# Optimization experiments

Measured on AMD Instinct MI355X. Metric: run time of the kernel, lower is better.

Reference implementation:

```python
import jax, jax.numpy as jnp
import numpy as np

B, C, HW, P = 8, 128, 50176, 128  # batch, channels, flattened spatial, num parcels

def setup_inputs() -> dict:
    key = jax.random.key(0)
    k1, k2 = jax.random.split(key)
    x = jax.random.normal(k1, (B, C, HW), dtype=jnp.float32)
    # 0/1 parcel assignment mask [b, num_parcs, hw]
    parcel_mask_batch = jax.random.randint(k2, (B, P, HW), 0, 2).astype(jnp.float32)
    return {"x": x, "parcel_mask_batch": parcel_mask_batch}

def reference(x, parcel_mask_batch):
    # torch: for each i, x[i] @ mask[i].T  -> stacked [b, c, num_parcs]
    # out[b, c, p] = sum_hw x[b, c, hw] * mask[b, p, hw]
    return jnp.einsum('bch,bph->bcp', x, parcel_mask_batch)
```

## Files before the change

### kernel.cpp

```cpp
#include <hip/hip_runtime.h>
#include <hip/hip_bf16.h>

typedef float f32x4 __attribute__((ext_vector_type(4)));
typedef short short8 __attribute__((ext_vector_type(8)));

#define BATCH 8
#define CH    128
#define HWN   50176
#define PN    128
#define KSPLIT 32
#define KWIN  1568
#define BK    224
#define NST   7
#define NKS   49

__device__ __forceinline__ ushort f2bf_rn(float f){
  uint u = __float_as_uint(f);
  u += 0x7FFFu + ((u >> 16) & 1u);
  return (ushort)(u >> 16);
}
__device__ __forceinline__ float bf2f(ushort h){
  return __uint_as_float(((uint)h) << 16);
}

__device__ __forceinline__ short8 cvt8_trunc(f32x4 a, f32x4 b){
  union{ short8 v; ushort u[8]; } r;
  r.u[0]=(ushort)(__float_as_uint(a.x)>>16); r.u[1]=(ushort)(__float_as_uint(a.y)>>16);
  r.u[2]=(ushort)(__float_as_uint(a.z)>>16); r.u[3]=(ushort)(__float_as_uint(a.w)>>16);
  r.u[4]=(ushort)(__float_as_uint(b.x)>>16); r.u[5]=(ushort)(__float_as_uint(b.y)>>16);
  r.u[6]=(ushort)(__float_as_uint(b.z)>>16); r.u[7]=(ushort)(__float_as_uint(b.w)>>16);
  return r.v;
}

__device__ __forceinline__ void cvt8_hilo(f32x4 a, f32x4 b, short8& h8, short8& l8){
  union{ short8 v; ushort u[8]; } h, l;
  float f[8] = {a.x,a.y,a.z,a.w,b.x,b.y,b.z,b.w};
  #pragma unroll
  for(int j=0;j<8;++j){
    ushort hh = (ushort)(__float_as_uint(f[j]) >> 16);
    h.u[j] = hh;
    l.u[j] = f2bf_rn(f[j] - bf2f(hh));
  }
  h8 = h.v; l8 = l.v;
}

template<int EPI>
__global__ __launch_bounds__(512, 1)
void raggr_kernel(const float* __restrict__ X, const float* __restrict__ Mk,
                  float* __restrict__ OUT, float* __restrict__ PART){
  __shared__ char smem[2 * 65536];

  const int tid  = threadIdx.x;
  const int b    = blockIdx.x >> 5;
  const int s    = blockIdx.x & 31;
  const int lane = tid & 63;
  const int w    = tid >> 6;
  const int l15  = lane & 15;
  const int hi4  = lane >> 4;

  const size_t base = (size_t)b * CH * HWN + (size_t)s * KWIN;
  const f32x4 z4 = {0.f,0.f,0.f,0.f};

  const float* pX = X + base + (size_t)(w*16 + l15) * HWN + hi4*8;

  const int mr = tid >> 2;
  const int mc = tid & 3;
  const int r7 = mr & 7;
  const float* pM = Mk + base + (size_t)mr * HWN + mc*56;
  char* mwr = smem + mr*512;

  f32x4 acc[8];
  #pragma unroll
  for(int n=0;n<8;++n) acc[n] = z4;

  f32x4 xr[4][2];
  f32x4 mreg[14];

  #define ISSUE_X(g) {                                                        \
    xr[(g)&3][0] = *(const f32x4*)(pX + (size_t)(g)*32);                      \
    xr[(g)&3][1] = *(const f32x4*)(pX + (size_t)(g)*32 + 4);                  \
  }
  #define ISSUE_M(t) {                                                        \
    _Pragma("unroll")                                                         \
    for(int i=0;i<14;++i)                                                     \
      mreg[i] = *(const f32x4*)(pM + (size_t)(t)*BK + i*4);                   \
  }
  #define CVTW_M(buf) {                                                      \
    char* dst = mwr + (buf)*65536;                                            \
    _Pragma("unroll")                                                         \
    for(int i=0;i<7;++i){                                                     \
      short8 v = cvt8_trunc(mreg[2*i], mreg[2*i+1]);                          \
      *(short8*)(dst + (((mc*7 + i) ^ r7) << 4)) = v;                         \
    } }

  ISSUE_M(0);
  ISSUE_X(0); ISSUE_X(1); ISSUE_X(2); ISSUE_X(3);
  CVTW_M(0);
  ISSUE_M(1);
  __syncthreads();

  #pragma unroll
  for(int g=0; g<NKS; ++g){
    const int t  = g / 7;
    const int ks = g % 7;
    const char* Mb = smem + (t & 1) * 65536;

    short8 bf[8];
    #pragma unroll
    for(int n=0;n<8;++n){
      int p = n*16 + l15;
      bf[n] = *(const short8*)(Mb + p*512 + (((ks*4 + hi4) ^ (p & 7)) << 4));
    }
    short8 ah, al;
    cvt8_hilo(xr[g&3][0], xr[g&3][1], ah, al);

    #pragma unroll
    for(int n=0;n<8;++n){
      acc[n] = __builtin_amdgcn_mfma_f32_16x16x32_bf16(ah, bf[n], acc[n], 0,0,0);
      acc[n] = __builtin_amdgcn_mfma_f32_16x16x32_bf16(al, bf[n], acc[n], 0,0,0);
    }

    if(g + 4 < NKS) ISSUE_X(g + 4);

    if(ks == 6 && t < NST-1){
      CVTW_M((t+1) & 1);
      if(t < NST-2) ISSUE_M(t+2);
      __syncthreads();
    }
  }

  if(EPI == 0){
    #pragma unroll
    for(int n=0;n<8;++n){
      int col  = n*16 + l15;
      int row0 = w*16 + hi4*4;
      #pragma unroll
      for(int j=0;j<4;++j)
        PART[(size_t)b*524288 + (size_t)(row0+j)*4096 + s*128 + col] = acc[n][j];
    }
  } else {
    float* o = OUT + (size_t)b * 16384;
    #pragma unroll
    for(int n=0;n<8;++n){
      int col  = n*16 + l15;
      int row0 = w*16 + hi4*4;
      #pragma unroll
      for(int j=0;j<4;++j) atomicAdd(&o[(size_t)(row0+j)*128 + col], acc[n][j]);
    }
  }
  #undef ISSUE_X
  #undef ISSUE_M
  #undef CVTW_M
}

__global__ void reduce_kernel(const float* __restrict__ PART, float* __restrict__ OUT){
  int bid = blockIdx.x;
  int b   = bid >> 6;
  int c   = (bid & 63)*2 + (threadIdx.x >> 7);
  int p   = threadIdx.x & 127;
  size_t base_ = (size_t)b*524288 + (size_t)c*4096 + p;
  float sum = 0.f;
  #pragma unroll 8
  for(int k=0;k<32;++k) sum += PART[base_ + k*128];
  OUT[(size_t)b*16384 + c*128 + p] = sum;
}

__global__ void zero_kernel(float* __restrict__ OUT){
  int idx = blockIdx.x * 256 + threadIdx.x;
  if(idx < BATCH*CH*PN) OUT[idx] = 0.f;
}

extern "C" void kernel_launch(void* const* d_in, const int* in_sizes, int n_in,
                              void* d_out, int out_size, void* d_ws, size_t ws_size,
                              hipStream_t stream){
  const float* X  = (const float*)d_in[0];
  const float* Mk = (const float*)d_in[1];
  float* O = (float*)d_out;

  const size_t part_bytes = (size_t)BATCH * KSPLIT * CH * PN * sizeof(float);
  if(ws_size >= part_bytes && d_ws != nullptr){
    float* part = (float*)d_ws;
    raggr_kernel<0><<<dim3(BATCH*KSPLIT), dim3(512), 0, stream>>>(X, Mk, O, part);
    reduce_kernel<<<dim3(512), dim3(256), 0, stream>>>(part, O);
  } else {
    zero_kernel<<<dim3(512), dim3(256), 0, stream>>>(O);
    raggr_kernel<1><<<dim3(BATCH*KSPLIT), dim3(512), 0, stream>>>(X, Mk, O, nullptr);
  }
}
```

Before: 411.9 us.

## Pack parcel mask into bitmasks and stage X hi/lo bf16 in LDS

The mask tile is no longer stored as bf16 in shared memory. It is compressed into 32-bit ballot bitmasks, and the MFMA B operands are rebuilt from those bits at compute time. X is now staged through LDS as packed hi/lo bf16 pairs using a single-buffer load/compute loop, and the launch bounds allow two blocks per CU. The goal is to shrink the LDS footprint enough for higher occupancy and to cut the LDS traffic for the mask. In exchange it adds ALU work for bit expansion and uses scalar strided mask loads. The bitmask path is only exact because the mask is 0/1.

```diff
diff --git a/kernel.cpp b/kernel.cpp
--- a/kernel.cpp
+++ b/kernel.cpp
@@ -2,6 +2,8 @@
 #include <hip/hip_bf16.h>
 
 typedef float f32x4 __attribute__((ext_vector_type(4)));
+typedef unsigned int u32;
+typedef u32 u32x4 __attribute__((ext_vector_type(4)));
 typedef short short8 __attribute__((ext_vector_type(8)));
 
 #define BATCH 8
@@ -12,43 +14,19 @@
 #define KWIN  1568
 #define BK    224
 #define NST   7
-#define NKS   49
 
 __device__ __forceinline__ ushort f2bf_rn(float f){
-  uint u = __float_as_uint(f);
+  u32 u = __float_as_uint(f);
   u += 0x7FFFu + ((u >> 16) & 1u);
   return (ushort)(u >> 16);
 }
-__device__ __forceinline__ float bf2f(ushort h){
-  return __uint_as_float(((uint)h) << 16);
-}
-
-__device__ __forceinline__ short8 cvt8_trunc(f32x4 a, f32x4 b){
-  union{ short8 v; ushort u[8]; } r;
-  r.u[0]=(ushort)(__float_as_uint(a.x)>>16); r.u[1]=(ushort)(__float_as_uint(a.y)>>16);
-  r.u[2]=(ushort)(__float_as_uint(a.z)>>16); r.u[3]=(ushort)(__float_as_uint(a.w)>>16);
-  r.u[4]=(ushort)(__float_as_uint(b.x)>>16); r.u[5]=(ushort)(__float_as_uint(b.y)>>16);
-  r.u[6]=(ushort)(__float_as_uint(b.z)>>16); r.u[7]=(ushort)(__float_as_uint(b.w)>>16);
-  return r.v;
-}
-
-__device__ __forceinline__ void cvt8_hilo(f32x4 a, f32x4 b, short8& h8, short8& l8){
-  union{ short8 v; ushort u[8]; } h, l;
-  float f[8] = {a.x,a.y,a.z,a.w,b.x,b.y,b.z,b.w};
-  #pragma unroll
-  for(int j=0;j<8;++j){
-    ushort hh = (ushort)(__float_as_uint(f[j]) >> 16);
-    h.u[j] = hh;
-    l.u[j] = f2bf_rn(f[j] - bf2f(hh));
-  }
-  h8 = h.v; l8 = l.v;
-}
 
 template<int EPI>
-__global__ __launch_bounds__(512, 1)
+__global__ __launch_bounds__(512, 2)
 void raggr_kernel(const float* __restrict__ X, const float* __restrict__ Mk,
                   float* __restrict__ OUT, float* __restrict__ PART){
-  __shared__ char smem[2 * 65536];
+  __shared__ u32 xtile[128*256];
+  __shared__ u32 mbits[128*7];
 
   const int tid  = threadIdx.x;
   const int b    = blockIdx.x >> 5;
@@ -59,74 +37,89 @@
   const int hi4  = lane >> 4;
 
   const size_t base = (size_t)b * CH * HWN + (size_t)s * KWIN;
-  const f32x4 z4 = {0.f,0.f,0.f,0.f};
 
-  const float* pX = X + base + (size_t)(w*16 + l15) * HWN + hi4*8;
+  const int xrow = w*16 + (lane >> 2);
+  const int xc   = lane & 3;
+  const float* pXs = X + base + (size_t)xrow * HWN + xc*56;
+  u32* xw = xtile + xrow*256;
+  const int rx15 = xrow & 15;
 
-  const int mr = tid >> 2;
-  const int mc = tid & 3;
-  const int r7 = mr & 7;
-  const float* pM = Mk + base + (size_t)mr * HWN + mc*56;
-  char* mwr = smem + mr*512;
+  const float* pMs = Mk + base + (size_t)(w*16 + (lane >> 5)) * HWN + (lane & 31);
 
+  const int arow = w*16 + l15;
+  const u32* xrd = xtile + arow*256;
+  const int ra15 = arow & 15;
+
+  f32x4 xv[14];
+  float mv[56];
   f32x4 acc[8];
   #pragma unroll
-  for(int n=0;n<8;++n) acc[n] = z4;
+  for(int n=0;n<8;++n) acc[n] = (f32x4){0.f,0.f,0.f,0.f};
 
-  f32x4 xr[4][2];
-  f32x4 mreg[14];
+  #define XISSUE(t) { _Pragma("unroll")                                       \
+    for(int i=0;i<14;++i)                                                     \
+      xv[i] = *(const f32x4*)(pXs + (size_t)(t)*BK + i*4); }
 
-  #define ISSUE_X(g) {                                                        \
-    xr[(g)&3][0] = *(const f32x4*)(pX + (size_t)(g)*32);                      \
-    xr[(g)&3][1] = *(const f32x4*)(pX + (size_t)(g)*32 + 4);                  \
-  }
-  #define ISSUE_M(t) {                                                        \
-    _Pragma("unroll")                                                         \
-    for(int i=0;i<14;++i)                                                     \
-      mreg[i] = *(const f32x4*)(pM + (size_t)(t)*BK + i*4);                   \
-  }
-  #define CVTW_M(buf) {                                                      \
-    char* dst = mwr + (buf)*65536;                                            \
-    _Pragma("unroll")                                                         \
-    for(int i=0;i<7;++i){                                                     \
-      short8 v = cvt8_trunc(mreg[2*i], mreg[2*i+1]);                          \
-      *(short8*)(dst + (((mc*7 + i) ^ r7) << 4)) = v;                         \
+  #define MISSUE(t) { _Pragma("unroll")                                       \
+    for(int i=0;i<56;++i)                                                     \
+      mv[i] = *(const float*)(pMs + (size_t)(2*(i/7))*HWN + (size_t)(t)*BK + (i%7)*32); }
+
+  #define XWRITE() { _Pragma("unroll")                                        \
+    for(int i=0;i<14;++i){                                                    \
+      u32x4 wd;                                                               \
+      _Pragma("unroll")                                                       \
+      for(int j=0;j<4;++j){                                                   \
+        float f = xv[i][j];                                                   \
+        u32 uu = __float_as_uint(f);                                          \
+        u32 hb = uu & 0xFFFF0000u;                                            \
+        wd[j] = hb | (u32)f2bf_rn(f - __uint_as_float(hb));                   \
+      }                                                                       \
+      *(u32x4*)(xw + (((xc*14 + i) ^ rx15) << 2)) = wd;                       \
     } }
 
-  ISSUE_M(0);
-  ISSUE_X(0); ISSUE_X(1); ISSUE_X(2); ISSUE_X(3);
-  CVTW_M(0);
-  ISSUE_M(1);
-  __syncthreads();
+  #define MWRITE() { _Pragma("unroll")                                        \
+    for(int i=0;i<56;++i){                                                    \
+      unsigned long long bal = __ballot(mv[i] != 0.0f);                       \
+      if((lane & 31) == 0)                                                    \
+        mbits[(w*16 + 2*(i/7) + (lane>>5))*7 + (i%7)] = (u32)(bal >> ((lane>>5)*32)); \
+    } }
 
-  #pragma unroll
-  for(int g=0; g<NKS; ++g){
-    const int t  = g / 7;
-    const int ks = g % 7;
-    const char* Mb = smem + (t & 1) * 65536;
+  #define COMPUTE() { _Pragma("unroll")                                       \
+    for(int ks=0;ks<7;++ks){                                                  \
+      u32x4 w0 = *(const u32x4*)(xrd + (((ks*8 + hi4*2    ) ^ ra15) << 2));   \
+      u32x4 w1 = *(const u32x4*)(xrd + (((ks*8 + hi4*2 + 1) ^ ra15) << 2));   \
+      union{ short8 v; u32 u[4]; } ah, al;                                    \
+      ah.u[0] = (w0[0]>>16) | (w0[1]&0xFFFF0000u);  al.u[0] = (w0[0]&0xFFFFu) | (w0[1]<<16); \
+      ah.u[1] = (w0[2]>>16) | (w0[3]&0xFFFF0000u);  al.u[1] = (w0[2]&0xFFFFu) | (w0[3]<<16); \
+      ah.u[2] = (w1[0]>>16) | (w1[1]&0xFFFF0000u);  al.u[2] = (w1[0]&0xFFFFu) | (w1[1]<<16); \
+      ah.u[3] = (w1[2]>>16) | (w1[3]&0xFFFF0000u);  al.u[3] = (w1[2]&0xFFFFu) | (w1[3]<<16); \
+      _Pragma("unroll")                                                       \
+      for(int n=0;n<8;++n){                                                   \
+        u32 byt = (mbits[(n*16+l15)*7 + ks] >> (hi4*8)) & 0xFFu;              \
+        union{ short8 v; u32 u[4]; } bfr;                                     \
+        _Pragma("unroll")                                                     \
+        for(int j=0;j<4;++j){                                                 \
+          u32 t2 = byt >> (2*j);                                              \
+          bfr.u[j] = ((t2 & 1u) ? 0x00003F80u : 0u) | ((t2 & 2u) ? 0x3F800000u : 0u); \
+        }                                                                     \
+        acc[n] = __builtin_amdgcn_mfma_f32_16x16x32_bf16(ah.v, bfr.v, acc[n], 0,0,0); \
+        acc[n] = __builtin_amdgcn_mfma_f32_16x16x32_bf16(al.v, bfr.v, acc[n], 0,0,0); \
+      }                                                                       \
+    } }
 
-    short8 bf[8];
-    #pragma unroll
-    for(int n=0;n<8;++n){
-      int p = n*16 + l15;
-      bf[n] = *(const short8*)(Mb + p*512 + (((ks*4 + hi4) ^ (p & 7)) << 4));
-    }
-    short8 ah, al;
-    cvt8_hilo(xr[g&3][0], xr[g&3][1], ah, al);
+  XISSUE(0); MISSUE(0);
 
-    #pragma unroll
-    for(int n=0;n<8;++n){
-      acc[n] = __builtin_amdgcn_mfma_f32_16x16x32_bf16(ah, bf[n], acc[n], 0,0,0);
-      acc[n] = __builtin_amdgcn_mfma_f32_16x16x32_bf16(al, bf[n], acc[n], 0,0,0);
-    }
-
-    if(g + 4 < NKS) ISSUE_X(g + 4);
-
-    if(ks == 6 && t < NST-1){
-      CVTW_M((t+1) & 1);
-      if(t < NST-2) ISSUE_M(t+2);
-      __syncthreads();
-    }
+  #pragma unroll 1
+  for(int t=0; t<NST; ++t){
+    XWRITE();
+    MWRITE();
+    if(t+1 < NST){ XISSUE(t+1); MISSUE(t+1); }
+    asm volatile("s_waitcnt lgkmcnt(0)" ::: "memory");
+    __builtin_amdgcn_s_barrier();
+    __builtin_amdgcn_sched_barrier(0);
+    COMPUTE();
+    __builtin_amdgcn_s_barrier();
+    __builtin_amdgcn_sched_barrier(0);
   }
 
   if(EPI == 0){
@@ -148,9 +141,11 @@
       for(int j=0;j<4;++j) atomicAdd(&o[(size_t)(row0+j)*128 + col], acc[n][j]);
     }
   }
-  #undef ISSUE_X
-  #undef ISSUE_M
-  #undef CVTW_M
+  #undef XISSUE
+  #undef MISSUE
+  #undef XWRITE
+  #undef MWRITE
+  #undef COMPUTE
 }
 
 __global__ void reduce_kernel(const float* __restrict__ PART, float* __restrict__ OUT){
```

Result: slower. 429.6 us (+4.3%).

## Double split-K to 64 with smaller LDS tiles and higher occupancy

Applied to the files above, without the earlier changes.

Doubles the K split from 32 to 64 slices, so each block handles a 784-wide window in 112-element stages using a 64KB LDS double buffer instead of 128KB. This allows up to four blocks per CU under the raised launch bounds and creates 512 blocks instead of 256, improving latency hiding and CU fill. The 112-wide stage does not divide evenly into 32-wide MFMA steps, so the last step of each stage zero-pads half the lanes. This wastes some MFMA work, and the partial buffer and its reduction pass become twice as large. Barriers become explicit s_waitcnt plus s_barrier with sched_barrier, and B fragments are loaded per MFMA rather than all up front.

```diff
diff --git a/kernel.cpp b/kernel.cpp
--- a/kernel.cpp
+++ b/kernel.cpp
@@ -2,25 +2,22 @@
 #include <hip/hip_bf16.h>
 
 typedef float f32x4 __attribute__((ext_vector_type(4)));
+typedef unsigned int u32;
 typedef short short8 __attribute__((ext_vector_type(8)));
 
 #define BATCH 8
 #define CH    128
 #define HWN   50176
 #define PN    128
-#define KSPLIT 32
-#define KWIN  1568
-#define BK    224
+#define KSPLIT 64
+#define KWIN  784
+#define BK    112
 #define NST   7
-#define NKS   49
 
 __device__ __forceinline__ ushort f2bf_rn(float f){
-  uint u = __float_as_uint(f);
+  u32 u = __float_as_uint(f);
   u += 0x7FFFu + ((u >> 16) & 1u);
   return (ushort)(u >> 16);
-}
-__device__ __forceinline__ float bf2f(ushort h){
-  return __uint_as_float(((uint)h) << 16);
 }
 
 __device__ __forceinline__ short8 cvt8_trunc(f32x4 a, f32x4 b){
@@ -37,22 +34,23 @@
   float f[8] = {a.x,a.y,a.z,a.w,b.x,b.y,b.z,b.w};
   #pragma unroll
   for(int j=0;j<8;++j){
-    ushort hh = (ushort)(__float_as_uint(f[j]) >> 16);
+    u32 uu = __float_as_uint(f[j]);
+    ushort hh = (ushort)(uu >> 16);
     h.u[j] = hh;
-    l.u[j] = f2bf_rn(f[j] - bf2f(hh));
+    l.u[j] = f2bf_rn(f[j] - __uint_as_float((u32)hh << 16));
   }
   h8 = h.v; l8 = l.v;
 }
 
 template<int EPI>
-__global__ __launch_bounds__(512, 1)
+__global__ __launch_bounds__(512, 4)
 void raggr_kernel(const float* __restrict__ X, const float* __restrict__ Mk,
                   float* __restrict__ OUT, float* __restrict__ PART){
-  __shared__ char smem[2 * 65536];
+  __shared__ char mlds[2 * 32768];
 
   const int tid  = threadIdx.x;
-  const int b    = blockIdx.x >> 5;
-  const int s    = blockIdx.x & 31;
+  const int b    = blockIdx.x >> 6;
+  const int s    = blockIdx.x & 63;
   const int lane = tid & 63;
   const int w    = tid >> 6;
   const int l15  = lane & 15;
@@ -61,71 +59,78 @@
   const size_t base = (size_t)b * CH * HWN + (size_t)s * KWIN;
   const f32x4 z4 = {0.f,0.f,0.f,0.f};
 
-  const float* pX = X + base + (size_t)(w*16 + l15) * HWN + hi4*8;
+  const int arow = w*16 + l15;
+  const float* pXb = X + base + (size_t)arow * HWN;
+  const int xo  = hi4 * 8;
+  const int xo3 = (hi4 < 2) ? hi4*8 : 8;
 
   const int mr = tid >> 2;
   const int mc = tid & 3;
+  const float* pMs = Mk + base + (size_t)mr * HWN + mc*32;
   const int r7 = mr & 7;
-  const float* pM = Mk + base + (size_t)mr * HWN + mc*56;
-  char* mwr = smem + mr*512;
 
+  f32x4 xr[4][2];
+  f32x4 mreg[8];
   f32x4 acc[8];
   #pragma unroll
   for(int n=0;n<8;++n) acc[n] = z4;
 
-  f32x4 xr[4][2];
-  f32x4 mreg[14];
+  #define XISSUE(g) {                                                         \
+    const int t_=(g)>>2, j_=(g)&3;                                            \
+    const size_t o_ = (size_t)(t_*112 + (j_<3 ? j_*32 + xo : 96 + xo3));      \
+    xr[(g)&3][0] = *(const f32x4*)(pXb + o_);                                 \
+    xr[(g)&3][1] = *(const f32x4*)(pXb + o_ + 4); }
 
-  #define ISSUE_X(g) {                                                        \
-    xr[(g)&3][0] = *(const f32x4*)(pX + (size_t)(g)*32);                      \
-    xr[(g)&3][1] = *(const f32x4*)(pX + (size_t)(g)*32 + 4);                  \
-  }
-  #define ISSUE_M(t) {                                                        \
+  #define MISSUE(t) { _Pragma("unroll")                                       \
+    for(int i=0;i<8;++i){                                                     \
+      if(i<4 || mc<3)                                                         \
+        mreg[i] = *(const f32x4*)(pMs + (size_t)(t)*BK + i*4); } }
+
+  #define CVTW(t) {                                                           \
+    char* dst = mlds + ((t)&1)*32768 + mr*256;                                \
     _Pragma("unroll")                                                         \
-    for(int i=0;i<14;++i)                                                     \
-      mreg[i] = *(const f32x4*)(pM + (size_t)(t)*BK + i*4);                   \
-  }
-  #define CVTW_M(buf) {                                                      \
-    char* dst = mwr + (buf)*65536;                                            \
-    _Pragma("unroll")                                                         \
-    for(int i=0;i<7;++i){                                                     \
-      short8 v = cvt8_trunc(mreg[2*i], mreg[2*i+1]);                          \
-      *(short8*)(dst + (((mc*7 + i) ^ r7) << 4)) = v;                         \
-    } }
+    for(int u=0;u<4;++u){                                                     \
+      if(u<2 || mc<3){                                                        \
+        short8 v = cvt8_trunc(mreg[2*u], mreg[2*u+1]);                        \
+        *(short8*)(dst + ((((mc<<2)+u) ^ r7) << 4)) = v;                      \
+      } } }
 
-  ISSUE_M(0);
-  ISSUE_X(0); ISSUE_X(1); ISSUE_X(2); ISSUE_X(3);
-  CVTW_M(0);
-  ISSUE_M(1);
-  __syncthreads();
+  XISSUE(0); XISSUE(1); XISSUE(2); XISSUE(3);
+  MISSUE(0);
+  CVTW(0);
+  MISSUE(1);
+  asm volatile("s_waitcnt lgkmcnt(0)" ::: "memory");
+  __builtin_amdgcn_s_barrier();
+  __builtin_amdgcn_sched_barrier(0);
 
   #pragma unroll
-  for(int g=0; g<NKS; ++g){
-    const int t  = g / 7;
-    const int ks = g % 7;
-    const char* Mb = smem + (t & 1) * 65536;
+  for(int g=0; g<NST*4; ++g){
+    const int t_ = g >> 2;
+    const int j_ = g & 3;
+    const char* Mb = mlds + (t_ & 1)*32768;
 
-    short8 bf[8];
+    f32x4 v0 = xr[g&3][0], v1 = xr[g&3][1];
+    if(j_ == 3 && hi4 >= 2){ v0 = z4; v1 = z4; }
+    short8 ah, al;
+    cvt8_hilo(v0, v1, ah, al);
+
+    const int unit = (j_ < 3) ? (j_*4 + hi4) : (12 + ((hi4 < 2) ? hi4 : 1));
     #pragma unroll
     for(int n=0;n<8;++n){
-      int p = n*16 + l15;
-      bf[n] = *(const short8*)(Mb + p*512 + (((ks*4 + hi4) ^ (p & 7)) << 4));
-    }
-    short8 ah, al;
-    cvt8_hilo(xr[g&3][0], xr[g&3][1], ah, al);
-
-    #pragma unroll
-    for(int n=0;n<8;++n){
-      acc[n] = __builtin_amdgcn_mfma_f32_16x16x32_bf16(ah, bf[n], acc[n], 0,0,0);
-      acc[n] = __builtin_amdgcn_mfma_f32_16x16x32_bf16(al, bf[n], acc[n], 0,0,0);
+      const int p = n*16 + l15;
+      short8 bf = *(const short8*)(Mb + p*256 + ((unit ^ (p & 7)) << 4));
+      acc[n] = __builtin_amdgcn_mfma_f32_16x16x32_bf16(ah, bf, acc[n], 0,0,0);
+      acc[n] = __builtin_amdgcn_mfma_f32_16x16x32_bf16(al, bf, acc[n], 0,0,0);
     }
 
-    if(g + 4 < NKS) ISSUE_X(g + 4);
+    if(g + 4 < NST*4) XISSUE(g + 4);
 
-    if(ks == 6 && t < NST-1){
-      CVTW_M((t+1) & 1);
-      if(t < NST-2) ISSUE_M(t+2);
-      __syncthreads();
+    if(j_ == 3 && t_ < NST-1){
+      CVTW(t_ + 1);
+      if(t_ < NST-2) MISSUE(t_ + 2);
+      asm volatile("s_waitcnt lgkmcnt(0)" ::: "memory");
+      __builtin_amdgcn_s_barrier();
+      __builtin_amdgcn_sched_barrier(0);
     }
   }
 
@@ -136,7 +141,7 @@
       int row0 = w*16 + hi4*4;
       #pragma unroll
       for(int j=0;j<4;++j)
-        PART[(size_t)b*524288 + (size_t)(row0+j)*4096 + s*128 + col] = acc[n][j];
+        PART[(size_t)b*1048576 + (size_t)(row0+j)*8192 + s*128 + col] = acc[n][j];
     }
   } else {
     float* o = OUT + (size_t)b * 16384;
@@ -148,21 +153,21 @@
       for(int j=0;j<4;++j) atomicAdd(&o[(size_t)(row0+j)*128 + col], acc[n][j]);
     }
   }
-  #undef ISSUE_X
-  #undef ISSUE_M
-  #undef CVTW_M
+  #undef XISSUE
+  #undef MISSUE
+  #undef CVTW
 }
 
 __global__ void reduce_kernel(const float* __restrict__ PART, float* __restrict__ OUT){
-  int bid = blockIdx.x;
-  int b   = bid >> 6;
-  int c   = (bid & 63)*2 + (threadIdx.x >> 7);
-  int p   = threadIdx.x & 127;
-  size_t base_ = (size_t)b*524288 + (size_t)c*4096 + p;
+  int idx = blockIdx.x * 256 + threadIdx.x;
+  int p = idx & 127;
+  int c = (idx >> 7) & 127;
+  int b = idx >> 14;
+  size_t base_ = (size_t)b*1048576 + (size_t)c*8192 + p;
   float sum = 0.f;
   #pragma unroll 8
-  for(int k=0;k<32;++k) sum += PART[base_ + k*128];
-  OUT[(size_t)b*16384 + c*128 + p] = sum;
+  for(int s2=0; s2<KSPLIT; ++s2) sum += PART[base_ + (size_t)s2*128];
+  OUT[idx] = sum;
 }
 
 __global__ void zero_kernel(float* __restrict__ OUT){
```

Measured after the change: 436.3 us. 5.9% more time.
